# Performance work log

Hardware: AMD Instinct MI355X
Metric: run time of the kernel (lower is better)

## Reference

```python
import jax, jax.numpy as jnp
import numpy as np

NEG = -10000.0  # fp16-safe mask value, as in the torch module


def prelu(x, a):
    # nn.PReLU() default: single learnable slope shared across channels
    return jnp.where(x >= 0, x, a * x)


def setup_inputs() -> dict:
    key = jax.random.key(0)
    ks = jax.random.split(key, 9)
    B, L, D = 2048, 200, 128
    H1, H2 = 256, 128
    query = jax.random.normal(ks[0], (B, D), dtype=jnp.float32)
    keys = jax.random.normal(ks[1], (B, L, D), dtype=jnp.float32)
    mask = jax.random.randint(ks[2], (B, L), 0, 2, dtype=jnp.int32)
    s1 = 1.0 / np.sqrt(4 * D)
    s2 = 1.0 / np.sqrt(H1)
    s3 = 1.0 / np.sqrt(H2)
    W1 = jax.random.uniform(ks[3], (H1, 4 * D), minval=-s1, maxval=s1, dtype=jnp.float32)
    b1 = jax.random.uniform(ks[4], (H1,), minval=-s1, maxval=s1, dtype=jnp.float32)
    W2 = jax.random.uniform(ks[5], (H2, H1), minval=-s2, maxval=s2, dtype=jnp.float32)
    b2 = jax.random.uniform(ks[6], (H2,), minval=-s2, maxval=s2, dtype=jnp.float32)
    W3 = jax.random.uniform(ks[7], (1, H2), minval=-s3, maxval=s3, dtype=jnp.float32)
    b3 = jax.random.uniform(ks[8], (1,), minval=-s3, maxval=s3, dtype=jnp.float32)
    a1 = jnp.asarray(0.25, dtype=jnp.float32)  # PReLU init
    a2 = jnp.asarray(0.25, dtype=jnp.float32)
    return {"query": query, "keys": keys, "mask": mask,
            "W1": W1, "b1": b1, "a1": a1, "W2": W2, "b2": b2, "a2": a2,
            "W3": W3, "b3": b3}


def reference(query, keys, mask, W1, b1, a1, W2, b2, a2, W3, b3):
    B, L, D = keys.shape
    q = jnp.broadcast_to(query[:, None, :], (B, L, D))
    # [B, L, 4D] concat feature (query, key, diff, product)
    att_in = jnp.concatenate([q, keys, q - keys, q * keys], axis=-1)
    h = prelu(jnp.einsum('blf,hf->blh', att_in, W1) + b1, a1)
    h = prelu(jnp.einsum('blh,gh->blg', h, W2) + b2, a2)
    scores = (jnp.einsum('blg,og->blo', h, W3) + b3)[..., 0]  # [B, L]
    scores = jnp.where(mask == 0, NEG, scores)
    w = jax.nn.softmax(scores, axis=-1)
    w = jnp.where(mask == 0, 0.0, w)
    # weighted sum over history -> user interest [B, D]
    return jnp.einsum('bl,bld->bd', w, keys)
```

## Files before the change

kernel.cpp:

```cpp
#include <hip/hip_runtime.h>
#include <hip/hip_bf16.h>
#include <cstdint>

#define NEGV (-10000.0f)

typedef short bf16x8 __attribute__((ext_vector_type(8)));
typedef short bf16x4 __attribute__((ext_vector_type(4)));
typedef float f32x4 __attribute__((ext_vector_type(4)));

__device__ __forceinline__ short f2bf(float f) {
  union { float f; uint32_t u; } v; v.f = f;
  uint32_t u = v.u + 0x7fffu + ((v.u >> 16) & 1u);
  return (short)(u >> 16);
}
__device__ __forceinline__ float b2f(short s) {
  union { uint32_t u; float f; } v; v.u = ((uint32_t)(uint16_t)s) << 16;
  return v.f;
}
__device__ __forceinline__ uint32_t pk2(float lo, float hi) {
  union { __hip_bfloat162 h2; uint32_t u; } cv;
  cv.h2.x = __float2bfloat16(lo);
  cv.h2.y = __float2bfloat16(hi);
  return cv.u;
}

__device__ __forceinline__ void bar() {
  __builtin_amdgcn_sched_barrier(0);
  asm volatile("s_waitcnt lgkmcnt(0)" ::: "memory");
  __builtin_amdgcn_s_barrier();
  __builtin_amdgcn_sched_barrier(0);
}

__global__ void prep_weights(const float* __restrict__ W1, const float* __restrict__ W2,
                             short* __restrict__ Wk, short* __restrict__ Wd,
                             short* __restrict__ W2b) {
  int idx = blockIdx.x * 256 + threadIdx.x;
  if (idx < 32768) {
    int h = idx >> 7, d = idx & 127;
    Wk[idx] = f2bf(W1[h * 512 + 128 + d] - W1[h * 512 + 256 + d]);
  } else if (idx < 65536) {
    int i = idx - 32768;
    int h = i >> 7, d = i & 127;
    Wd[i] = f2bf(W1[h * 512 + 384 + d]);
  } else {
    int i = idx - 65536;
    W2b[i] = f2bf(W2[i]);
  }
}

__global__ void prep_u(const float* __restrict__ query, const float* __restrict__ W1,
                       const float* __restrict__ b1, float* __restrict__ U) {
  __shared__ float q8[8][128];
  int tid = threadIdx.x;
  int b0 = blockIdx.x * 8;
  for (int i = tid; i < 1024; i += 256)
    q8[i >> 7][i & 127] = query[(size_t)(b0 + (i >> 7)) * 128 + (i & 127)];
  __syncthreads();
  int h = tid;
  const float4* w0 = (const float4*)(W1 + (size_t)h * 512);
  const float4* w1 = (const float4*)(W1 + (size_t)h * 512 + 256);
  float acc[8];
  float bb = b1[h];
#pragma unroll
  for (int i = 0; i < 8; ++i) acc[i] = bb;
  for (int d4 = 0; d4 < 32; ++d4) {
    float4 wa = w0[d4], wb = w1[d4];
    float wv0 = wa.x + wb.x, wv1 = wa.y + wb.y, wv2 = wa.z + wb.z, wv3 = wa.w + wb.w;
#pragma unroll
    for (int i = 0; i < 8; ++i) {
      float4 qv = ((const float4*)q8[i])[d4];
      acc[i] += wv0 * qv.x + wv1 * qv.y + wv2 * qv.z + wv3 * qv.w;
    }
  }
#pragma unroll
  for (int i = 0; i < 8; ++i) U[(size_t)(b0 + i) * 256 + h] = acc[i];
}

__global__ __launch_bounds__(1024) void din_fused(
    const float* __restrict__ query, const float* __restrict__ keys,
    const int* __restrict__ mask,
    const float* __restrict__ b2p, const float* __restrict__ a1p,
    const float* __restrict__ a2p, const float* __restrict__ W3,
    const float* __restrict__ U, const short* __restrict__ Wk,
    const short* __restrict__ Wd, const short* __restrict__ W2b,
    float* __restrict__ out) {
  __shared__ short Kall[224 * 128];
  __shared__ short H1[2][32 * 256];
  __shared__ float wred[8][224];
  __shared__ float wl[224];
  __shared__ float red[16];
  __shared__ float opart[8][128];

  const int tid = threadIdx.x;
  const int b = blockIdx.x;
  const int lane = tid & 63, wid = tid >> 6;
  const int lr = lane & 15, lg = lane >> 4;
  const bool isG1 = wid < 8;
  const int sw = (lr & 7) << 3;

  bf16x8 frag[8];
  f32x4 accA, accB;
  float uv0[4], uv1[4];
  float alpha;

  if (isG1) {
    alpha = a1p[0];
    const float* qrow = query + (size_t)b * 128;
#pragma unroll
    for (int nt = 0; nt < 2; ++nt) {
      int h = wid * 32 + nt * 16 + lr;
#pragma unroll
      for (int ks = 0; ks < 4; ++ks) {
        int d0 = ks * 32 + lg * 8;
        bf16x8 wk = *(const bf16x8*)(Wk + h * 128 + d0);
        bf16x8 wd = *(const bf16x8*)(Wd + h * 128 + d0);
        float4 q0 = *(const float4*)(qrow + d0);
        float4 q1 = *(const float4*)(qrow + d0 + 4);
        float qv[8] = {q0.x, q0.y, q0.z, q0.w, q1.x, q1.y, q1.z, q1.w};
        float mv[8];
#pragma unroll
        for (int j = 0; j < 8; ++j) mv[j] = b2f(wk[j]) + b2f(wd[j]) * qv[j];
        union { bf16x8 v; uint32_t u[4]; } mm;
#pragma unroll
        for (int j = 0; j < 4; ++j) mm.u[j] = pk2(mv[2 * j], mv[2 * j + 1]);
        frag[nt * 4 + ks] = mm.v;
      }
    }
#pragma unroll
    for (int r = 0; r < 4; ++r) {
      uv0[r] = U[(size_t)b * 256 + wid * 32 + lg * 4 + r];
      uv1[r] = U[(size_t)b * 256 + wid * 32 + 16 + lg * 4 + r];
    }
  } else {
    alpha = a2p[0];
    int g = (wid - 8) * 16 + lr;
#pragma unroll
    for (int ks = 0; ks < 8; ++ks)
      frag[ks] = *(const bf16x8*)(W2b + g * 256 + ks * 32 + lg * 8);
#pragma unroll
    for (int r = 0; r < 4; ++r) {
      int gg = (wid - 8) * 16 + lg * 4 + r;
      uv0[r] = b2p[gg];
      uv1[r] = W3[gg];
    }
  }

  const int j = tid - 512;
  const int srow = j >> 4;
  const int scol = (j & 15) * 8;
  const int ssw = (srow & 7) << 3;

  float4 sa0, sa1, sb0, sb1;
  if (!isG1) {
#pragma unroll
    for (int t = 0; t < 2; ++t) {
      int row = t * 32 + srow;
      const float4* kp4 = (const float4*)(keys + ((size_t)b * 200 + row) * 128 + scol);
      float4 x0 = kp4[0], x1 = kp4[1];
      union { bf16x8 v; uint32_t u[4]; } w;
      w.u[0] = pk2(x0.x, x0.y); w.u[1] = pk2(x0.z, x0.w);
      w.u[2] = pk2(x1.x, x1.y); w.u[3] = pk2(x1.z, x1.w);
      *(bf16x8*)(&Kall[row * 128 + (scol ^ ssw)]) = w.v;
    }
    const float4* kp4 = (const float4*)(keys + ((size_t)b * 200 + 64 + srow) * 128 + scol);
    sa0 = kp4[0]; sa1 = kp4[1];
  }
  bar();

  for (int p = 0; p < 8; ++p) {
    const int buf = p & 1;

    if (isG1) {
      if (p < 7) {
#pragma unroll
        for (int s = 0; s < 2; ++s) {
          const int row = p * 32 + s * 16 + lr;
          bf16x8 kf[4];
#pragma unroll
          for (int ks = 0; ks < 4; ++ks)
            kf[ks] = *(const bf16x8*)(&Kall[row * 128 + ((ks * 32 + lg * 8) ^ sw)]);
#pragma unroll
          for (int r = 0; r < 4; ++r) { accA[r] = uv0[r]; accB[r] = uv1[r]; }
          __builtin_amdgcn_s_setprio(1);
#pragma unroll
          for (int ks = 0; ks < 4; ++ks) {
            accA = __builtin_amdgcn_mfma_f32_16x16x32_bf16(frag[ks], kf[ks], accA, 0, 0, 0);
            accB = __builtin_amdgcn_mfma_f32_16x16x32_bf16(frag[4 + ks], kf[ks], accB, 0, 0, 0);
          }
          __builtin_amdgcn_s_setprio(0);
          float v0, v1, v2, v3;
          union { bf16x4 v; uint32_t u[2]; } hh;
          short* h1row = &H1[buf][(s * 16 + lr) * 256];
          v0 = accA[0]; v1 = accA[1]; v2 = accA[2]; v3 = accA[3];
          v0 = (v0 >= 0.f) ? v0 : alpha * v0;
          v1 = (v1 >= 0.f) ? v1 : alpha * v1;
          v2 = (v2 >= 0.f) ? v2 : alpha * v2;
          v3 = (v3 >= 0.f) ? v3 : alpha * v3;
          hh.u[0] = pk2(v0, v1); hh.u[1] = pk2(v2, v3);
          *(bf16x4*)(&h1row[(wid * 32 + lg * 4) ^ sw]) = hh.v;
          v0 = accB[0]; v1 = accB[1]; v2 = accB[2]; v3 = accB[3];
          v0 = (v0 >= 0.f) ? v0 : alpha * v0;
          v1 = (v1 >= 0.f) ? v1 : alpha * v1;
          v2 = (v2 >= 0.f) ? v2 : alpha * v2;
          v3 = (v3 >= 0.f) ? v3 : alpha * v3;
          hh.u[0] = pk2(v0, v1); hh.u[1] = pk2(v2, v3);
          *(bf16x4*)(&h1row[(wid * 32 + 16 + lg * 4) ^ sw]) = hh.v;
        }
      }
    } else {
      const bool lv = (p + 3 <= 6);
      if (lv) {
        int gl = (p + 3) * 32 + srow;
        sb0 = sb1 = make_float4(0.f, 0.f, 0.f, 0.f);
        if (gl < 200) {
          const float4* kp4 = (const float4*)(keys + ((size_t)b * 200 + gl) * 128 + scol);
          sb0 = kp4[0]; sb1 = kp4[1];
        }
      }
      if (p >= 1) {
        const short* h1b = H1[buf ^ 1];
#pragma unroll
        for (int s = 0; s < 2; ++s) {
#pragma unroll
          for (int r = 0; r < 4; ++r) accA[r] = uv0[r];
          const short* hr = &h1b[(s * 16 + lr) * 256];
          __builtin_amdgcn_s_setprio(1);
#pragma unroll
          for (int ks = 0; ks < 8; ++ks) {
            bf16x8 hf = *(const bf16x8*)(&hr[(ks * 32 + lg * 8) ^ sw]);
            accA = __builtin_amdgcn_mfma_f32_16x16x32_bf16(frag[ks], hf, accA, 0, 0, 0);
          }
          __builtin_amdgcn_s_setprio(0);
          float sc = 0.f;
#pragma unroll
          for (int r = 0; r < 4; ++r) {
            float v = accA[r];
            v = (v >= 0.f) ? v : alpha * v;
            sc += v * uv1[r];
          }
          sc += __shfl_xor(sc, 16);
          sc += __shfl_xor(sc, 32);
          if (lg == 0) wred[wid - 8][(p - 1) * 32 + s * 16 + lr] = sc;
        }
      }
      if (p + 2 <= 6) {
        int row = (p + 2) * 32 + srow;
        union { bf16x8 v; uint32_t u[4]; } w;
        w.u[0] = pk2(sa0.x, sa0.y); w.u[1] = pk2(sa0.z, sa0.w);
        w.u[2] = pk2(sa1.x, sa1.y); w.u[3] = pk2(sa1.z, sa1.w);
        *(bf16x8*)(&Kall[row * 128 + (scol ^ ssw)]) = w.v;
      }
      if (lv) { sa0 = sb0; sa1 = sb1; }
    }
    bar();
  }

  if (tid < 224) {
    float s = 0.f;
#pragma unroll
    for (int w = 0; w < 8; ++w) s += wred[w][tid];
    wl[tid] = s;
  }
  bar();

  float val = NEGV;
  int mk = 0;
  if (tid < 200) {
    mk = mask[(size_t)b * 200 + tid];
    val = mk ? wl[tid] : NEGV;
  }
  float m = val;
#pragma unroll
  for (int off = 1; off < 64; off <<= 1) m = fmaxf(m, __shfl_xor(m, off));
  if (lane == 0) red[wid] = m;
  bar();
  float smax = red[0];
#pragma unroll
  for (int i = 1; i < 16; ++i) smax = fmaxf(smax, red[i]);
  float pex = (tid < 200 && mk) ? __expf(val - smax) : 0.f;
  float s = pex;
#pragma unroll
  for (int off = 1; off < 64; off <<= 1) s += __shfl_xor(s, off);
  bar();
  if (lane == 0) red[wid] = s;
  bar();
  float ssum = 0.f;
#pragma unroll
  for (int i = 0; i < 16; ++i) ssum += red[i];
  float winv = (ssum > 0.f) ? 1.f / ssum : 0.f;
  if (tid < 224) wl[tid] = (tid < 200) ? pex * winv : 0.f;
  bar();

  {
    const int d = tid & 127, slice = tid >> 7;
    float acc = 0.f;
    for (int l = slice; l < 200; l += 8) {
      float wv = wl[l];
      acc += wv * b2f(Kall[l * 128 + (d ^ ((l & 7) << 3))]);
    }
    opart[slice][d] = acc;
  }
  bar();
  if (tid < 128) {
    float acc = 0.f;
#pragma unroll
    for (int i = 0; i < 8; ++i) acc += opart[i][tid];
    out[(size_t)b * 128 + tid] = acc;
  }
}

extern "C" void kernel_launch(void* const* d_in, const int* in_sizes, int n_in,
                              void* d_out, int out_size, void* d_ws, size_t ws_size,
                              hipStream_t stream) {
  const float* query = (const float*)d_in[0];
  const float* keys  = (const float*)d_in[1];
  const int*   maskp = (const int*)d_in[2];
  const float* W1    = (const float*)d_in[3];
  const float* b1    = (const float*)d_in[4];
  const float* a1    = (const float*)d_in[5];
  const float* W2    = (const float*)d_in[6];
  const float* b2    = (const float*)d_in[7];
  const float* a2    = (const float*)d_in[8];
  const float* W3    = (const float*)d_in[9];
  float* out = (float*)d_out;

  float* U   = (float*)d_ws;
  short* Wk  = (short*)((char*)d_ws + 2097152);
  short* Wd  = Wk + 32768;
  short* W2b = Wd + 32768;

  prep_weights<<<384, 256, 0, stream>>>(W1, W2, Wk, Wd, W2b);
  prep_u<<<256, 256, 0, stream>>>(query, W1, b1, U);
  din_fused<<<2048, 1024, 0, stream>>>(query, keys, maskp, b2, a1, a2, W3,
                                       U, Wk, Wd, W2b, out);
}
```

Measured before the change: 165.9 us.

## Double the pipeline stage to 64 rows and spread key loading across all waves

The fused DIN kernel now processes 64 history rows per pipeline stage instead of 32. That cuts the loop from 8 to 5 iterations and removes three block-wide barriers. Key staging from global memory into LDS as bf16 is now shared by all 1024 threads rather than only the second-layer waves, so each thread does fewer loads and conversions. The cost is more LDS (Kall, H1, wred and wl all grow) and more padded zero rows (256 vs 224). The first-layer waves now also carry global-load latency inside their stage.

```diff
diff --git a/kernel.cpp b/kernel.cpp
--- a/kernel.cpp
+++ b/kernel.cpp
@@ -84,10 +84,10 @@
     const float* __restrict__ U, const short* __restrict__ Wk,
     const short* __restrict__ Wd, const short* __restrict__ W2b,
     float* __restrict__ out) {
-  __shared__ short Kall[224 * 128];
-  __shared__ short H1[2][32 * 256];
-  __shared__ float wred[8][224];
-  __shared__ float wl[224];
+  __shared__ short Kall[256 * 128];
+  __shared__ short H1[2][64 * 256];
+  __shared__ float wred[8][256];
+  __shared__ float wl[256];
   __shared__ float red[16];
   __shared__ float opart[8][128];
 
@@ -145,16 +145,14 @@
     }
   }
 
-  const int j = tid - 512;
-  const int srow = j >> 4;
-  const int scol = (j & 15) * 8;
+  const int srow = tid >> 4;
+  const int scol = (tid & 15) * 8;
   const int ssw = (srow & 7) << 3;
 
-  float4 sa0, sa1, sb0, sb1;
-  if (!isG1) {
+  {
 #pragma unroll
     for (int t = 0; t < 2; ++t) {
-      int row = t * 32 + srow;
+      int row = t * 64 + srow;
       const float4* kp4 = (const float4*)(keys + ((size_t)b * 200 + row) * 128 + scol);
       float4 x0 = kp4[0], x1 = kp4[1];
       union { bf16x8 v; uint32_t u[4]; } w;
@@ -162,19 +160,28 @@
       w.u[2] = pk2(x1.x, x1.y); w.u[3] = pk2(x1.z, x1.w);
       *(bf16x8*)(&Kall[row * 128 + (scol ^ ssw)]) = w.v;
     }
-    const float4* kp4 = (const float4*)(keys + ((size_t)b * 200 + 64 + srow) * 128 + scol);
-    sa0 = kp4[0]; sa1 = kp4[1];
-  }
-  bar();
-
-  for (int p = 0; p < 8; ++p) {
+  }
+  bar();
+
+  for (int p = 0; p < 5; ++p) {
     const int buf = p & 1;
 
+    float4 r0, r1;
+    const bool lv = (p < 2);
+    if (lv) {
+      int row = (p + 2) * 64 + srow;
+      r0 = r1 = make_float4(0.f, 0.f, 0.f, 0.f);
+      if (row < 200) {
+        const float4* kp4 = (const float4*)(keys + ((size_t)b * 200 + row) * 128 + scol);
+        r0 = kp4[0]; r1 = kp4[1];
+      }
+    }
+
     if (isG1) {
-      if (p < 7) {
-#pragma unroll
-        for (int s = 0; s < 2; ++s) {
-          const int row = p * 32 + s * 16 + lr;
+      if (p < 4) {
+#pragma unroll
+        for (int s = 0; s < 4; ++s) {
+          const int row = p * 64 + s * 16 + lr;
           bf16x8 kf[4];
 #pragma unroll
           for (int ks = 0; ks < 4; ++ks)
@@ -208,19 +215,10 @@
         }
       }
     } else {
-      const bool lv = (p + 3 <= 6);
-      if (lv) {
-        int gl = (p + 3) * 32 + srow;
-        sb0 = sb1 = make_float4(0.f, 0.f, 0.f, 0.f);
-        if (gl < 200) {
-          const float4* kp4 = (const float4*)(keys + ((size_t)b * 200 + gl) * 128 + scol);
-          sb0 = kp4[0]; sb1 = kp4[1];
-        }
-      }
       if (p >= 1) {
         const short* h1b = H1[buf ^ 1];
 #pragma unroll
-        for (int s = 0; s < 2; ++s) {
+        for (int s = 0; s < 4; ++s) {
 #pragma unroll
           for (int r = 0; r < 4; ++r) accA[r] = uv0[r];
           const short* hr = &h1b[(s * 16 + lr) * 256];
@@ -240,22 +238,22 @@
           }
           sc += __shfl_xor(sc, 16);
           sc += __shfl_xor(sc, 32);
-          if (lg == 0) wred[wid - 8][(p - 1) * 32 + s * 16 + lr] = sc;
+          if (lg == 0) wred[wid - 8][(p - 1) * 64 + s * 16 + lr] = sc;
         }
       }
-      if (p + 2 <= 6) {
-        int row = (p + 2) * 32 + srow;
-        union { bf16x8 v; uint32_t u[4]; } w;
-        w.u[0] = pk2(sa0.x, sa0.y); w.u[1] = pk2(sa0.z, sa0.w);
-        w.u[2] = pk2(sa1.x, sa1.y); w.u[3] = pk2(sa1.z, sa1.w);
-        *(bf16x8*)(&Kall[row * 128 + (scol ^ ssw)]) = w.v;
-      }
-      if (lv) { sa0 = sb0; sa1 = sb1; }
+    }
+
+    if (lv) {
+      int row = (p + 2) * 64 + srow;
+      union { bf16x8 v; uint32_t u[4]; } w;
+      w.u[0] = pk2(r0.x, r0.y); w.u[1] = pk2(r0.z, r0.w);
+      w.u[2] = pk2(r1.x, r1.y); w.u[3] = pk2(r1.z, r1.w);
+      *(bf16x8*)(&Kall[row * 128 + (scol ^ ssw)]) = w.v;
     }
     bar();
   }
 
-  if (tid < 224) {
+  if (tid < 256) {
     float s = 0.f;
 #pragma unroll
     for (int w = 0; w < 8; ++w) s += wred[w][tid];
@@ -288,7 +286,7 @@
 #pragma unroll
   for (int i = 0; i < 16; ++i) ssum += red[i];
   float winv = (ssum > 0.f) ? 1.f / ssum : 0.f;
-  if (tid < 224) wl[tid] = (tid < 200) ? pex * winv : 0.f;
+  if (tid < 256) wl[tid] = (tid < 200) ? pex * winv : 0.f;
   bar();
 
   {
```

Result: slower. 175.6 us (+5.8%).
